# Optimization experiments

Hardware: AMD Instinct MI355X
Metric: run time of the kernel (lower is better)

The kernel has to match this reference:

```python
import jax, jax.numpy as jnp
import numpy as np

N_HEAD = 8
HEAD_DIM = 64
DIM = 512
INNER = N_HEAD * HEAD_DIM
ATT_THRESHOLD = 1e-4
SCALE = HEAD_DIM ** -0.5


def setup_inputs() -> dict:
    key = jax.random.key(0)
    ks = jax.random.split(key, 7)
    b, n, dn = 2, 2048, 2048
    fr = jax.random.normal(ks[0], (b, n, DIM), dtype=jnp.float32)
    dt = jax.random.normal(ks[1], (b, dn, DIM), dtype=jnp.float32)
    s = DIM ** -0.5
    Wq = jax.random.normal(ks[2], (DIM, INNER), dtype=jnp.float32) * s
    Wk = jax.random.normal(ks[3], (DIM, INNER), dtype=jnp.float32) * s
    Wv = jax.random.normal(ks[4], (DIM, INNER), dtype=jnp.float32) * s
    Wo = jax.random.normal(ks[5], (INNER, DIM), dtype=jnp.float32) * (INNER ** -0.5)
    bo = jax.random.normal(ks[6], (DIM,), dtype=jnp.float32) * 0.01
    return {"fr": fr, "dt": dt, "Wq": Wq, "Wk": Wk, "Wv": Wv, "Wo": Wo, "bo": bo}


def reference(fr, dt, Wq, Wk, Wv, Wo, bo):
    b, n, _ = fr.shape
    dn = dt.shape[1]
    # projections -> [b, seq, n_head, head_dim]
    q = (fr @ Wq).reshape(b, n, N_HEAD, HEAD_DIM)
    k = (dt @ Wk).reshape(b, dn, N_HEAD, HEAD_DIM)
    v = (dt @ Wv).reshape(b, dn, N_HEAD, HEAD_DIM)
    # full attention matrix [b, h, n, dn]
    scores = jnp.einsum('bihd,bjhd->bhij', q, k) * SCALE
    attn = jax.nn.softmax(scores, axis=-1)
    # torch .clip(t) with one positional arg clamps the MIN: max(attn, t)
    attn = jnp.maximum(attn, ATT_THRESHOLD) - ATT_THRESHOLD
    attn = attn / jnp.sum(attn, axis=-1, keepdims=True)
    out = jnp.einsum('bhij,bjhd->bihd', attn, v).reshape(b, n, INNER)
    return out @ Wo + bo
```

## Files before the change

### kernel.cpp

```cpp
#include <hip/hip_runtime.h>
#include <hip/hip_bf16.h>

#define BB 2
#define SEQ 2048
#define NHEAD 8
#define HD 64
#define ATT_T 1e-4f
#define QSCALE 0.18033688011112042f

typedef short s16x8 __attribute__((ext_vector_type(8)));
typedef float f32x16 __attribute__((ext_vector_type(16)));

#define MFMA32(a, b, c) __builtin_amdgcn_mfma_f32_32x32x16_bf16((a), (b), (c), 0, 0, 0)
#define EXP2(x) __builtin_amdgcn_exp2f(x)
#define SB0() __builtin_amdgcn_sched_barrier(0)
#define WAITVM0() __builtin_amdgcn_s_waitcnt(0x0F70)
#define WAITVM4() __builtin_amdgcn_s_waitcnt(0x0F74)
#define WAITVM8() __builtin_amdgcn_s_waitcnt(0x0F78)

__device__ __forceinline__ unsigned short bfr(float x) {
  __hip_bfloat16 h = __float2bfloat16(x);
  return __builtin_bit_cast(unsigned short, h);
}
__device__ __forceinline__ unsigned int packbf(float a, float b) {
  return (unsigned int)bfr(a) | ((unsigned int)bfr(b) << 16);
}
__device__ __forceinline__ unsigned int permpack(float a, float b) {
  return __builtin_amdgcn_perm(__builtin_bit_cast(unsigned int, b),
                               __builtin_bit_cast(unsigned int, a), 0x07060302u);
}
__device__ __forceinline__ void async16(const void* g, void* l) {
  __builtin_amdgcn_global_load_lds(
      (const __attribute__((address_space(1))) unsigned int*)g,
      (__attribute__((address_space(3))) unsigned int*)l, 16, 0, 0);
}

__global__ __launch_bounds__(256) void convT(const float* __restrict__ w0,
                                             const float* __restrict__ w1,
                                             const float* __restrict__ w2,
                                             const float* __restrict__ w3,
                                             unsigned short* __restrict__ o0,
                                             unsigned short* __restrict__ o1,
                                             unsigned short* __restrict__ o2,
                                             unsigned short* __restrict__ o3) {
  __shared__ float tle[64][65];
  const float* W = blockIdx.z == 0 ? w0 : blockIdx.z == 1 ? w1 : blockIdx.z == 2 ? w2 : w3;
  unsigned short* WT = blockIdx.z == 0 ? o0 : blockIdx.z == 1 ? o1 : blockIdx.z == 2 ? o2 : o3;
  const int r0 = blockIdx.y * 64, c0 = blockIdx.x * 64;
  const int tr = threadIdx.x >> 4;
  const int tc = threadIdx.x & 15;
  #pragma unroll
  for (int i = 0; i < 4; i++) {
    int r = tr + i * 16;
    float4 v = *(const float4*)(W + (size_t)(r0 + r) * 512 + c0 + tc * 4);
    tle[r][tc * 4 + 0] = v.x;
    tle[r][tc * 4 + 1] = v.y;
    tle[r][tc * 4 + 2] = v.z;
    tle[r][tc * 4 + 3] = v.w;
  }
  __syncthreads();
  #pragma unroll
  for (int i = 0; i < 4; i++) {
    int c = tr + i * 16;
    int rr = tc * 4;
    uint2 p;
    p.x = packbf(tle[rr + 0][c], tle[rr + 1][c]);
    p.y = packbf(tle[rr + 2][c], tle[rr + 3][c]);
    *(uint2*)(WT + (size_t)(c0 + c) * 512 + r0 + rr) = p;
  }
}

__global__ __launch_bounds__(256) void gemm_qkv(const float* __restrict__ frF,
                                                const float* __restrict__ dtF,
                                                const unsigned short* __restrict__ WqT,
                                                const unsigned short* __restrict__ WkT,
                                                const unsigned short* __restrict__ WvT,
                                                unsigned short* __restrict__ Qp,
                                                unsigned short* __restrict__ Kp,
                                                unsigned short* __restrict__ VTp) {
  __shared__ __align__(16) unsigned short smem[24576];
  unsigned short* Asm = smem;
  unsigned short* Bsm = smem + 8192;
  const int tid = threadIdx.x, lane = tid & 63, w = tid >> 6;
  const int l31 = lane & 31, lh = lane >> 5;
  const int m0 = blockIdx.y * 64, n0 = blockIdx.x * 128;
  const int z = blockIdx.z;
  const float* A = z == 0 ? frF : dtF;
  const unsigned short* BT = z == 0 ? WqT : (z == 1 ? WkT : WvT);
  unsigned short* OP = z == 0 ? Qp : (z == 1 ? Kp : VTp);
  const float scale = z == 0 ? QSCALE : 1.0f;

  const int arow = tid >> 2, aseg = tid & 3;
  const float* Ap = A + (size_t)(m0 + arow) * 512 + aseg * 16;
  const int aoff = (arow >> 5) * 2048 + aseg * 512 + (arow & 31) * 8;

  auto stageB = [&](int kt, int buf) {
    const int k0 = kt * 64;
    #pragma unroll
    for (int i = 0; i < 4; i++) {
      int r = w * 4 + i, gn = r >> 2, ks = r & 3;
      async16(BT + (size_t)(n0 + gn * 32 + l31) * 512 + k0 + ks * 16 + lh * 8,
              Bsm + buf * 8192 + r * 512);
    }
  };
  auto ldA = [&](int kt, float4* r4) {
    #pragma unroll
    for (int i = 0; i < 4; i++) r4[i] = *(const float4*)(Ap + kt * 64 + i * 4);
  };
  auto wrA = [&](int buf, const float4* r4) {
    uint4 w0v, w1v;
    w0v.x = packbf(r4[0].x, r4[0].y); w0v.y = packbf(r4[0].z, r4[0].w);
    w0v.z = packbf(r4[1].x, r4[1].y); w0v.w = packbf(r4[1].z, r4[1].w);
    w1v.x = packbf(r4[2].x, r4[2].y); w1v.y = packbf(r4[2].z, r4[2].w);
    w1v.z = packbf(r4[3].x, r4[3].y); w1v.w = packbf(r4[3].z, r4[3].w);
    *(uint4*)(Asm + buf * 4096 + aoff) = w0v;
    *(uint4*)(Asm + buf * 4096 + aoff + 256) = w1v;
  };

  f32x16 acc[2];
  #pragma unroll
  for (int j = 0; j < 2; j++)
    #pragma unroll
    for (int r = 0; r < 16; r++) acc[j][r] = 0.f;

  float4 areg[4];
  ldA(0, areg);
  stageB(0, 0);
  wrA(0, areg);
  ldA(1, areg);

  for (int kt = 0; kt < 8; ++kt) {
    __syncthreads();
    if (kt + 1 < 8) {
      const int nb = (kt + 1) & 1;
      stageB(kt + 1, nb);
      wrA(nb, areg);
      if (kt + 2 < 8) ldA(kt + 2, areg);
    }
    const int buf = kt & 1;
    const unsigned short* as = Asm + buf * 4096 + (w & 1) * 2048;
    const unsigned short* bs = Bsm + buf * 8192 + (w >> 1) * 4096;
    #pragma unroll
    for (int ks = 0; ks < 4; ++ks) {
      s16x8 af = *(const s16x8*)(as + ks * 512 + lane * 8);
      s16x8 b0 = *(const s16x8*)(bs + ks * 512 + lane * 8);
      s16x8 b1 = *(const s16x8*)(bs + 2048 + ks * 512 + lane * 8);
      acc[0] = MFMA32(af, b0, acc[0]);
      acc[1] = MFMA32(af, b1, acc[1]);
    }
  }

  const int wm = (w & 1) * 32, wn = (w >> 1) * 64;
  const int bb = m0 >> 11, s0 = m0 & 2047;
  __syncthreads();
  if (z <= 1) {
    #pragma unroll
    for (int j = 0; j < 2; j++)
      #pragma unroll
      for (int r = 0; r < 16; r++) {
        int mm = wm + (r & 3) + 8 * (r >> 2) + 4 * lh;
        int nn = wn + j * 32 + l31;
        smem[mm * 136 + nn] = bfr(acc[j][r] * scale);
      }
    __syncthreads();
    #pragma unroll
    for (int it = 0; it < 4; ++it) {
      int c = tid + it * 256;
      int mm = c >> 4, seg = c & 15;
      uint4 vdat = *(const uint4*)(smem + mm * 136 + seg * 8);
      int n = n0 + seg * 8, h = n >> 6, d = n & 63;
      *(uint4*)(OP + ((size_t)((bb * NHEAD + h) * SEQ + s0 + mm)) * HD + d) = vdat;
    }
  } else {
    #pragma unroll
    for (int j = 0; j < 2; j++)
      #pragma unroll
      for (int r = 0; r < 16; r += 2) {
        int mm = wm + (r & 3) + 8 * (r >> 2) + 4 * lh;
        int nn = wn + j * 32 + l31;
        *(unsigned int*)(smem + nn * 72 + mm) = packbf(acc[j][r], acc[j][r + 1]);
      }
    __syncthreads();
    #pragma unroll
    for (int it = 0; it < 4; ++it) {
      int c = tid + it * 256;
      int nn = c >> 3, seg = c & 7;
      uint4 vdat = *(const uint4*)(smem + nn * 72 + seg * 8);
      int n = n0 + nn, h = n >> 6, d = n & 63;
      *(uint4*)(OP + ((size_t)((bb * NHEAD + h) * HD + d)) * SEQ + s0 + seg * 8) = vdat;
    }
  }
}

__global__ __launch_bounds__(256) void gemm_out(const unsigned short* __restrict__ A,
                                                const unsigned short* __restrict__ BT,
                                                const float* __restrict__ bias,
                                                float* __restrict__ O) {
  __shared__ __align__(16) unsigned short smem[16384];
  unsigned short* Asm = smem;
  unsigned short* Bsm = smem + 8192;
  const int tid = threadIdx.x, lane = tid & 63, w = tid >> 6;
  const int l31 = lane & 31, lh = lane >> 5;
  const int m0 = blockIdx.y * 64, n0 = blockIdx.x * 64;

  auto stage = [&](int kt, int buf) {
    const int k0 = kt * 64;
    #pragma unroll
    for (int i = 0; i < 2; i++) {
      int r = w * 2 + i, g = r >> 2, ks = r & 3;
      async16(A + (size_t)(m0 + g * 32 + l31) * 512 + k0 + ks * 16 + lh * 8,
              Asm + buf * 4096 + r * 512);
      async16(BT + (size_t)(n0 + g * 32 + l31) * 512 + k0 + ks * 16 + lh * 8,
              Bsm + buf * 4096 + r * 512);
    }
  };

  f32x16 acc;
  #pragma unroll
  for (int r = 0; r < 16; r++) acc[r] = 0.f;

  stage(0, 0);
  for (int kt = 0; kt < 8; ++kt) {
    __syncthreads();
    if (kt + 1 < 8) stage(kt + 1, (kt + 1) & 1);
    const int buf = kt & 1;
    const unsigned short* as = Asm + buf * 4096 + (w & 1) * 2048;
    const unsigned short* bs = Bsm + buf * 4096 + (w >> 1) * 2048;
    #pragma unroll
    for (int ks = 0; ks < 4; ++ks) {
      s16x8 af = *(const s16x8*)(as + ks * 512 + lane * 8);
      s16x8 bf = *(const s16x8*)(bs + ks * 512 + lane * 8);
      acc = MFMA32(af, bf, acc);
    }
  }

  const int wm = (w & 1) * 32, wn = (w >> 1) * 32;
  float bv = bias[n0 + wn + l31];
  #pragma unroll
  for (int r = 0; r < 16; r++) {
    int mm = wm + (r & 3) + 8 * (r >> 2) + 4 * lh;
    O[(size_t)(m0 + mm) * 512 + n0 + wn + l31] = acc[r] + bv;
  }
}

__global__ __launch_bounds__(256, 2) void attn_mfma(const unsigned short* __restrict__ Q,
                                                    const unsigned short* __restrict__ K,
                                                    const unsigned short* __restrict__ VT,
                                                    unsigned short* __restrict__ O) {
  __shared__ __align__(16) unsigned short arena[4][8192];
  __shared__ float larr[4][64];
  __shared__ float warr[4][64];

  const int tid = threadIdx.x;
  const int lane = tid & 63;
  const int w = tid >> 6;
  const int l31 = lane & 31, lh = lane >> 5;

  const int bid = blockIdx.x;
  const int g = bid & 7, j = bid >> 3;
  const int bh = g * 2 + (j >> 5);
  const int qt = j & 31;

  const unsigned short* Qh = Q + (size_t)bh * SEQ * HD;
  const unsigned short* Kh = K + (size_t)bh * SEQ * HD;
  const unsigned short* VTh = VT + (size_t)bh * HD * SEQ;

  s16x8 qf[2][4];
  #pragma unroll
  for (int q2 = 0; q2 < 2; q2++)
    #pragma unroll
    for (int t = 0; t < 4; t++)
      qf[q2][t] = *(const s16x8*)(Qh + (size_t)(qt * 64 + q2 * 32 + l31) * HD + 16 * t + 8 * lh);

  unsigned short* kbuf = &arena[w][0];
  unsigned short* vbuf = &arena[w][4096];
  const int kbase = w * 512;

  auto stageK = [&](int c, int slot) {
    const unsigned short* base = Kh + (size_t)(kbase + c * 32 + l31) * HD + lh * 8;
    #pragma unroll
    for (int tt = 0; tt < 4; tt++)
      async16(base + tt * 16, kbuf + slot * 2048 + tt * 512);
  };
  auto stageV = [&](int c, int slot) {
    #pragma unroll
    for (int dh = 0; dh < 2; dh++)
      #pragma unroll
      for (int kc = 0; kc < 2; kc++)
        async16(VTh + (size_t)(dh * 32 + l31) * SEQ + kbase + c * 32 + kc * 16 + lh * 8,
                vbuf + slot * 2048 + (dh * 2 + kc) * 512);
  };

  float lsum[2] = {0.f, 0.f};
  f32x16 scp[2];

  auto accum_l = [&]() {
    #pragma unroll
    for (int q2 = 0; q2 < 2; q2++) {
      float s0 = 0.f, s1 = 0.f, s2 = 0.f, s3 = 0.f;
      #pragma unroll
      for (int r = 0; r < 4; r++) {
        s0 += EXP2(scp[q2][r]);
        s1 += EXP2(scp[q2][4 + r]);
        s2 += EXP2(scp[q2][8 + r]);
        s3 += EXP2(scp[q2][12 + r]);
      }
      lsum[q2] += (s0 + s1) + (s2 + s3);
    }
  };

  stageK(0, 0);
  for (int c = 0; c < 16; ++c) {
    const int slot = c & 1;
    if (c + 1 < 16) stageK(c + 1, slot ^ 1);
    if (c > 0) accum_l();
    if (c + 1 < 16) { WAITVM4(); } else { WAITVM0(); }
    SB0();
    s16x8 kf[4];
    #pragma unroll
    for (int tt = 0; tt < 4; tt++)
      kf[tt] = *(const s16x8*)(kbuf + slot * 2048 + tt * 512 + lane * 8);
    #pragma unroll
    for (int q2 = 0; q2 < 2; q2++) {
      f32x16 sc;
      #pragma unroll
      for (int r = 0; r < 16; r++) sc[r] = 0.f;
      #pragma unroll
      for (int tt = 0; tt < 4; tt++) sc = MFMA32(kf[tt], qf[q2][tt], sc);
      scp[q2] = sc;
    }
  }
  accum_l();
  #pragma unroll
  for (int q2 = 0; q2 < 2; q2++) lsum[q2] += __shfl_xor(lsum[q2], 32);
  if (lh == 0) { larr[w][l31] = lsum[0]; larr[w][32 + l31] = lsum[1]; }
  __syncthreads();
  float tl[2];
  #pragma unroll
  for (int q2 = 0; q2 < 2; q2++)
    tl[q2] = ATT_T * (larr[0][q2 * 32 + l31] + larr[1][q2 * 32 + l31] +
                      larr[2][q2 * 32 + l31] + larr[3][q2 * 32 + l31]);

  f32x16 acc[2][2];
  #pragma unroll
  for (int q2 = 0; q2 < 2; q2++)
    #pragma unroll
    for (int dh = 0; dh < 2; dh++)
      #pragma unroll
      for (int r = 0; r < 16; r++) acc[q2][dh][r] = 0.f;
  float wacc[2] = {0.f, 0.f};
  s16x8 vfp[2][2];

  auto softmax_pv = [&]() {
    s16x8 pf[2][2];
    #pragma unroll
    for (int q2 = 0; q2 < 2; q2++) {
      uint2 quads[4];
      #pragma unroll
      for (int gq = 0; gq < 4; gq++) {
        float u0 = fmaxf(EXP2(scp[q2][4 * gq + 0]) - tl[q2], 0.f);
        float u1 = fmaxf(EXP2(scp[q2][4 * gq + 1]) - tl[q2], 0.f);
        float u2 = fmaxf(EXP2(scp[q2][4 * gq + 2]) - tl[q2], 0.f);
        float u3 = fmaxf(EXP2(scp[q2][4 * gq + 3]) - tl[q2], 0.f);
        wacc[q2] += (u0 + u1) + (u2 + u3);
        quads[gq].x = permpack(u0, u1);
        quads[gq].y = permpack(u2, u3);
      }
      #pragma unroll
      for (int tp = 0; tp < 2; tp++) {
        uint2 ea, eb;
        ea.x = (unsigned)__shfl_xor((int)quads[2 * tp].x, 32);
        ea.y = (unsigned)__shfl_xor((int)quads[2 * tp].y, 32);
        eb.x = (unsigned)__shfl_xor((int)quads[2 * tp + 1].x, 32);
        eb.y = (unsigned)__shfl_xor((int)quads[2 * tp + 1].y, 32);
        uint4 fr;
        if (lh == 0) { fr.x = quads[2 * tp].x; fr.y = quads[2 * tp].y; fr.z = ea.x; fr.w = ea.y; }
        else         { fr.x = eb.x; fr.y = eb.y; fr.z = quads[2 * tp + 1].x; fr.w = quads[2 * tp + 1].y; }
        pf[q2][tp] = __builtin_bit_cast(s16x8, fr);
      }
    }
    #pragma unroll
    for (int q2 = 0; q2 < 2; q2++)
      #pragma unroll
      for (int dh = 0; dh < 2; dh++) {
        acc[q2][dh] = MFMA32(pf[q2][0], vfp[dh][0], acc[q2][dh]);
        acc[q2][dh] = MFMA32(pf[q2][1], vfp[dh][1], acc[q2][dh]);
      }
  };

  stageK(0, 0);
  stageV(0, 0);
  for (int c = 0; c < 16; ++c) {
    const int slot = c & 1;
    if (c + 1 < 16) { stageK(c + 1, slot ^ 1); stageV(c + 1, slot ^ 1); }
    if (c > 0) softmax_pv();
    if (c + 1 < 16) { WAITVM8(); } else { WAITVM0(); }
    SB0();
    s16x8 kf[4];
    #pragma unroll
    for (int tt = 0; tt < 4; tt++)
      kf[tt] = *(const s16x8*)(kbuf + slot * 2048 + tt * 512 + lane * 8);
    #pragma unroll
    for (int dh = 0; dh < 2; dh++)
      #pragma unroll
      for (int kc = 0; kc < 2; kc++)
        vfp[dh][kc] = *(const s16x8*)(vbuf + slot * 2048 + (dh * 2 + kc) * 512 + lane * 8);
    #pragma unroll
    for (int q2 = 0; q2 < 2; q2++) {
      f32x16 sc;
      #pragma unroll
      for (int r = 0; r < 16; r++) sc[r] = 0.f;
      #pragma unroll
      for (int tt = 0; tt < 4; tt++) sc = MFMA32(kf[tt], qf[q2][tt], sc);
      scp[q2] = sc;
    }
  }
  softmax_pv();

  #pragma unroll
  for (int q2 = 0; q2 < 2; q2++) wacc[q2] += __shfl_xor(wacc[q2], 32);
  if (lh == 0) { warr[w][l31] = wacc[0]; warr[w][32 + l31] = wacc[1]; }
  __syncthreads();

  float* plane0 = (float*)&arena[0][0];
  float* plane1 = (float*)&arena[2][0];

  if (w >= 2) {
    float* pl = (w == 2) ? plane0 : plane1;
    #pragma unroll
    for (int q2 = 0; q2 < 2; q2++)
      #pragma unroll
      for (int dh = 0; dh < 2; dh++)
        #pragma unroll
        for (int r = 0; r < 16; r++) {
          int ql = q2 * 32 + (r & 3) + 8 * (r >> 2) + 4 * lh;
          pl[ql * 64 + dh * 32 + l31] = acc[q2][dh][r];
        }
  }
  __syncthreads();
  if (w < 2) {
    float* pl = (w == 0) ? plane0 : plane1;
    #pragma unroll
    for (int q2 = 0; q2 < 2; q2++)
      #pragma unroll
      for (int dh = 0; dh < 2; dh++)
        #pragma unroll
        for (int r = 0; r < 16; r++) {
          int ql = q2 * 32 + (r & 3) + 8 * (r >> 2) + 4 * lh;
          acc[q2][dh][r] += pl[ql * 64 + dh * 32 + l31];
        }
  }
  __syncthreads();
  if (w == 1) {
    #pragma unroll
    for (int q2 = 0; q2 < 2; q2++)
      #pragma unroll
      for (int dh = 0; dh < 2; dh++)
        #pragma unroll
        for (int r = 0; r < 16; r++) {
          int ql = q2 * 32 + (r & 3) + 8 * (r >> 2) + 4 * lh;
          plane0[ql * 64 + dh * 32 + l31] = acc[q2][dh][r];
        }
  }
  __syncthreads();
  unsigned short* otile = &arena[2][0];
  if (w == 0) {
    #pragma unroll
    for (int q2 = 0; q2 < 2; q2++)
      #pragma unroll
      for (int dh = 0; dh < 2; dh++)
        #pragma unroll
        for (int r = 0; r < 16; r++) {
          int ql = q2 * 32 + (r & 3) + 8 * (r >> 2) + 4 * lh;
          float wt = warr[0][ql] + warr[1][ql] + warr[2][ql] + warr[3][ql];
          float v = (acc[q2][dh][r] + plane0[ql * 64 + dh * 32 + l31]) / wt;
          otile[ql * 64 + dh * 32 + l31] = bfr(v);
        }
  }
  __syncthreads();
  const int b = bh >> 3, h = bh & 7;
  #pragma unroll
  for (int it = 0; it < 2; ++it) {
    int c2 = tid + it * 256;
    int mm = c2 >> 3, seg = c2 & 7;
    uint4 vdat = *(const uint4*)(otile + mm * 64 + seg * 8);
    *(uint4*)(O + ((size_t)(b * SEQ + qt * 64 + mm)) * 512 + h * HD + seg * 8) = vdat;
  }
}

extern "C" void kernel_launch(void* const* d_in, const int* in_sizes, int n_in,
                              void* d_out, int out_size, void* d_ws, size_t ws_size,
                              hipStream_t stream) {
  const float* fr = (const float*)d_in[0];
  const float* dt = (const float*)d_in[1];
  const float* Wq = (const float*)d_in[2];
  const float* Wk = (const float*)d_in[3];
  const float* Wv = (const float*)d_in[4];
  const float* Wo = (const float*)d_in[5];
  const float* bo = (const float*)d_in[6];
  float* out = (float*)d_out;

  const size_t planeE = (size_t)BB * SEQ * 512;
  const size_t wE = 512 * 512;
  unsigned short* p = (unsigned short*)d_ws;
  unsigned short* WqT = p; p += wE;
  unsigned short* WkT = p; p += wE;
  unsigned short* WvT = p; p += wE;
  unsigned short* WoT = p; p += wE;
  unsigned short* Qp  = p; p += planeE;
  unsigned short* Kp  = p; p += planeE;
  unsigned short* VTp = p; p += planeE;
  unsigned short* aoB = p; p += planeE;

  convT<<<dim3(8, 8, 4), 256, 0, stream>>>(Wq, Wk, Wv, Wo, WqT, WkT, WvT, WoT);

  gemm_qkv<<<dim3(4, 64, 3), 256, 0, stream>>>(fr, dt, WqT, WkT, WvT, Qp, Kp, VTp);

  attn_mfma<<<BB * NHEAD * 32, 256, 0, stream>>>(Qp, Kp, VTp, aoB);

  gemm_out<<<dim3(8, 64), 256, 0, stream>>>(aoB, WoT, bo, out);
}
```

Before: 162.8 us.

## Halve attention query tile to 32 rows, single-buffer K/V, raise occupancy

The attention kernel now handles 32 query rows per block instead of 64, doubling the grid and shrinking per-wave accumulators and LDS to about half. The double-buffered K/V staging is replaced with one buffer: each iteration waits for the loads, reads fragments into registers, waits on LDS, then issues the next async load before the MFMA and softmax work. Launch bounds rise to 4 blocks per CU to gain occupancy and latency hiding. In exchange, K/V are re-read from global/L2 twice as often and the per-wave software pipeline gives way to inter-wave overlap.

```diff
diff --git a/kernel.cpp b/kernel.cpp
--- a/kernel.cpp
+++ b/kernel.cpp
@@ -14,9 +14,8 @@
 #define MFMA32(a, b, c) __builtin_amdgcn_mfma_f32_32x32x16_bf16((a), (b), (c), 0, 0, 0)
 #define EXP2(x) __builtin_amdgcn_exp2f(x)
 #define SB0() __builtin_amdgcn_sched_barrier(0)
-#define WAITVM0() __builtin_amdgcn_s_waitcnt(0x0F70)
-#define WAITVM4() __builtin_amdgcn_s_waitcnt(0x0F74)
-#define WAITVM8() __builtin_amdgcn_s_waitcnt(0x0F78)
+#define WAITVM0()   __builtin_amdgcn_s_waitcnt(0x0F70)
+#define WAITLGKM0() __builtin_amdgcn_s_waitcnt(0xC07F)
 
 __device__ __forceinline__ unsigned short bfr(float x) {
   __hip_bfloat16 h = __float2bfloat16(x);
@@ -243,13 +242,13 @@
   }
 }
 
-__global__ __launch_bounds__(256, 2) void attn_mfma(const unsigned short* __restrict__ Q,
+__global__ __launch_bounds__(256, 4) void attn_mfma(const unsigned short* __restrict__ Q,
                                                     const unsigned short* __restrict__ K,
                                                     const unsigned short* __restrict__ VT,
                                                     unsigned short* __restrict__ O) {
-  __shared__ __align__(16) unsigned short arena[4][8192];
-  __shared__ float larr[4][64];
-  __shared__ float warr[4][64];
+  __shared__ __align__(16) unsigned short arena[4][4096];
+  __shared__ float larr[4][32];
+  __shared__ float warr[4][32];
 
   const int tid = threadIdx.x;
   const int lane = tid & 63;
@@ -258,233 +257,185 @@
 
   const int bid = blockIdx.x;
   const int g = bid & 7, j = bid >> 3;
-  const int bh = g * 2 + (j >> 5);
-  const int qt = j & 31;
+  const int bh = g * 2 + (j >> 6);
+  const int qt = j & 63;
 
   const unsigned short* Qh = Q + (size_t)bh * SEQ * HD;
   const unsigned short* Kh = K + (size_t)bh * SEQ * HD;
   const unsigned short* VTh = VT + (size_t)bh * HD * SEQ;
 
-  s16x8 qf[2][4];
-  #pragma unroll
-  for (int q2 = 0; q2 < 2; q2++)
-    #pragma unroll
-    for (int t = 0; t < 4; t++)
-      qf[q2][t] = *(const s16x8*)(Qh + (size_t)(qt * 64 + q2 * 32 + l31) * HD + 16 * t + 8 * lh);
+  s16x8 qf[4];
+  #pragma unroll
+  for (int t = 0; t < 4; t++)
+    qf[t] = *(const s16x8*)(Qh + (size_t)(qt * 32 + l31) * HD + 16 * t + 8 * lh);
 
   unsigned short* kbuf = &arena[w][0];
-  unsigned short* vbuf = &arena[w][4096];
+  unsigned short* vbuf = &arena[w][2048];
   const int kbase = w * 512;
 
-  auto stageK = [&](int c, int slot) {
+  auto stageK = [&](int c) {
     const unsigned short* base = Kh + (size_t)(kbase + c * 32 + l31) * HD + lh * 8;
     #pragma unroll
     for (int tt = 0; tt < 4; tt++)
-      async16(base + tt * 16, kbuf + slot * 2048 + tt * 512);
-  };
-  auto stageV = [&](int c, int slot) {
+      async16(base + tt * 16, kbuf + tt * 512);
+  };
+  auto stageV = [&](int c) {
     #pragma unroll
     for (int dh = 0; dh < 2; dh++)
       #pragma unroll
       for (int kc = 0; kc < 2; kc++)
         async16(VTh + (size_t)(dh * 32 + l31) * SEQ + kbase + c * 32 + kc * 16 + lh * 8,
-                vbuf + slot * 2048 + (dh * 2 + kc) * 512);
-  };
-
-  float lsum[2] = {0.f, 0.f};
-  f32x16 scp[2];
-
-  auto accum_l = [&]() {
-    #pragma unroll
-    for (int q2 = 0; q2 < 2; q2++) {
-      float s0 = 0.f, s1 = 0.f, s2 = 0.f, s3 = 0.f;
-      #pragma unroll
-      for (int r = 0; r < 4; r++) {
-        s0 += EXP2(scp[q2][r]);
-        s1 += EXP2(scp[q2][4 + r]);
-        s2 += EXP2(scp[q2][8 + r]);
-        s3 += EXP2(scp[q2][12 + r]);
-      }
-      lsum[q2] += (s0 + s1) + (s2 + s3);
-    }
-  };
-
-  stageK(0, 0);
+                vbuf + (dh * 2 + kc) * 512);
+  };
+
+  float lsum = 0.f;
+  stageK(0);
   for (int c = 0; c < 16; ++c) {
-    const int slot = c & 1;
-    if (c + 1 < 16) stageK(c + 1, slot ^ 1);
-    if (c > 0) accum_l();
-    if (c + 1 < 16) { WAITVM4(); } else { WAITVM0(); }
+    WAITVM0();
     SB0();
     s16x8 kf[4];
     #pragma unroll
     for (int tt = 0; tt < 4; tt++)
-      kf[tt] = *(const s16x8*)(kbuf + slot * 2048 + tt * 512 + lane * 8);
-    #pragma unroll
-    for (int q2 = 0; q2 < 2; q2++) {
-      f32x16 sc;
-      #pragma unroll
-      for (int r = 0; r < 16; r++) sc[r] = 0.f;
-      #pragma unroll
-      for (int tt = 0; tt < 4; tt++) sc = MFMA32(kf[tt], qf[q2][tt], sc);
-      scp[q2] = sc;
-    }
-  }
-  accum_l();
-  #pragma unroll
-  for (int q2 = 0; q2 < 2; q2++) lsum[q2] += __shfl_xor(lsum[q2], 32);
-  if (lh == 0) { larr[w][l31] = lsum[0]; larr[w][32 + l31] = lsum[1]; }
-  __syncthreads();
-  float tl[2];
-  #pragma unroll
-  for (int q2 = 0; q2 < 2; q2++)
-    tl[q2] = ATT_T * (larr[0][q2 * 32 + l31] + larr[1][q2 * 32 + l31] +
-                      larr[2][q2 * 32 + l31] + larr[3][q2 * 32 + l31]);
-
-  f32x16 acc[2][2];
-  #pragma unroll
-  for (int q2 = 0; q2 < 2; q2++)
-    #pragma unroll
-    for (int dh = 0; dh < 2; dh++)
-      #pragma unroll
-      for (int r = 0; r < 16; r++) acc[q2][dh][r] = 0.f;
-  float wacc[2] = {0.f, 0.f};
-  s16x8 vfp[2][2];
-
-  auto softmax_pv = [&]() {
-    s16x8 pf[2][2];
-    #pragma unroll
-    for (int q2 = 0; q2 < 2; q2++) {
-      uint2 quads[4];
-      #pragma unroll
-      for (int gq = 0; gq < 4; gq++) {
-        float u0 = fmaxf(EXP2(scp[q2][4 * gq + 0]) - tl[q2], 0.f);
-        float u1 = fmaxf(EXP2(scp[q2][4 * gq + 1]) - tl[q2], 0.f);
-        float u2 = fmaxf(EXP2(scp[q2][4 * gq + 2]) - tl[q2], 0.f);
-        float u3 = fmaxf(EXP2(scp[q2][4 * gq + 3]) - tl[q2], 0.f);
-        wacc[q2] += (u0 + u1) + (u2 + u3);
-        quads[gq].x = permpack(u0, u1);
-        quads[gq].y = permpack(u2, u3);
-      }
-      #pragma unroll
-      for (int tp = 0; tp < 2; tp++) {
-        uint2 ea, eb;
-        ea.x = (unsigned)__shfl_xor((int)quads[2 * tp].x, 32);
-        ea.y = (unsigned)__shfl_xor((int)quads[2 * tp].y, 32);
-        eb.x = (unsigned)__shfl_xor((int)quads[2 * tp + 1].x, 32);
-        eb.y = (unsigned)__shfl_xor((int)quads[2 * tp + 1].y, 32);
-        uint4 fr;
-        if (lh == 0) { fr.x = quads[2 * tp].x; fr.y = quads[2 * tp].y; fr.z = ea.x; fr.w = ea.y; }
-        else         { fr.x = eb.x; fr.y = eb.y; fr.z = quads[2 * tp + 1].x; fr.w = quads[2 * tp + 1].y; }
-        pf[q2][tp] = __builtin_bit_cast(s16x8, fr);
-      }
-    }
-    #pragma unroll
-    for (int q2 = 0; q2 < 2; q2++)
-      #pragma unroll
-      for (int dh = 0; dh < 2; dh++) {
-        acc[q2][dh] = MFMA32(pf[q2][0], vfp[dh][0], acc[q2][dh]);
-        acc[q2][dh] = MFMA32(pf[q2][1], vfp[dh][1], acc[q2][dh]);
-      }
-  };
-
-  stageK(0, 0);
-  stageV(0, 0);
+      kf[tt] = *(const s16x8*)(kbuf + tt * 512 + lane * 8);
+    WAITLGKM0();
+    SB0();
+    if (c + 1 < 16) stageK(c + 1);
+    f32x16 sc;
+    #pragma unroll
+    for (int r = 0; r < 16; r++) sc[r] = 0.f;
+    #pragma unroll
+    for (int tt = 0; tt < 4; tt++) sc = MFMA32(kf[tt], qf[tt], sc);
+    float s0 = 0.f, s1 = 0.f, s2 = 0.f, s3 = 0.f;
+    #pragma unroll
+    for (int r = 0; r < 4; r++) {
+      s0 += EXP2(sc[r]);
+      s1 += EXP2(sc[4 + r]);
+      s2 += EXP2(sc[8 + r]);
+      s3 += EXP2(sc[12 + r]);
+    }
+    lsum += (s0 + s1) + (s2 + s3);
+  }
+  lsum += __shfl_xor(lsum, 32);
+  if (lh == 0) larr[w][l31] = lsum;
+  __syncthreads();
+  const float tl = ATT_T * (larr[0][l31] + larr[1][l31] + larr[2][l31] + larr[3][l31]);
+
+  f32x16 acc[2];
+  #pragma unroll
+  for (int dh = 0; dh < 2; dh++)
+    #pragma unroll
+    for (int r = 0; r < 16; r++) acc[dh][r] = 0.f;
+  float wacc = 0.f;
+
+  stageK(0);
+  stageV(0);
   for (int c = 0; c < 16; ++c) {
-    const int slot = c & 1;
-    if (c + 1 < 16) { stageK(c + 1, slot ^ 1); stageV(c + 1, slot ^ 1); }
-    if (c > 0) softmax_pv();
-    if (c + 1 < 16) { WAITVM8(); } else { WAITVM0(); }
+    WAITVM0();
     SB0();
-    s16x8 kf[4];
+    s16x8 kf[4], vf[2][2];
     #pragma unroll
     for (int tt = 0; tt < 4; tt++)
-      kf[tt] = *(const s16x8*)(kbuf + slot * 2048 + tt * 512 + lane * 8);
+      kf[tt] = *(const s16x8*)(kbuf + tt * 512 + lane * 8);
     #pragma unroll
     for (int dh = 0; dh < 2; dh++)
       #pragma unroll
       for (int kc = 0; kc < 2; kc++)
-        vfp[dh][kc] = *(const s16x8*)(vbuf + slot * 2048 + (dh * 2 + kc) * 512 + lane * 8);
-    #pragma unroll
-    for (int q2 = 0; q2 < 2; q2++) {
-      f32x16 sc;
-      #pragma unroll
-      for (int r = 0; r < 16; r++) sc[r] = 0.f;
-      #pragma unroll
-      for (int tt = 0; tt < 4; tt++) sc = MFMA32(kf[tt], qf[q2][tt], sc);
-      scp[q2] = sc;
-    }
-  }
-  softmax_pv();
-
-  #pragma unroll
-  for (int q2 = 0; q2 < 2; q2++) wacc[q2] += __shfl_xor(wacc[q2], 32);
-  if (lh == 0) { warr[w][l31] = wacc[0]; warr[w][32 + l31] = wacc[1]; }
+        vf[dh][kc] = *(const s16x8*)(vbuf + (dh * 2 + kc) * 512 + lane * 8);
+    WAITLGKM0();
+    SB0();
+    if (c + 1 < 16) { stageK(c + 1); stageV(c + 1); }
+    f32x16 sc;
+    #pragma unroll
+    for (int r = 0; r < 16; r++) sc[r] = 0.f;
+    #pragma unroll
+    for (int tt = 0; tt < 4; tt++) sc = MFMA32(kf[tt], qf[tt], sc);
+    uint2 quads[4];
+    #pragma unroll
+    for (int gq = 0; gq < 4; gq++) {
+      float u0 = fmaxf(EXP2(sc[4 * gq + 0]) - tl, 0.f);
+      float u1 = fmaxf(EXP2(sc[4 * gq + 1]) - tl, 0.f);
+      float u2 = fmaxf(EXP2(sc[4 * gq + 2]) - tl, 0.f);
+      float u3 = fmaxf(EXP2(sc[4 * gq + 3]) - tl, 0.f);
+      wacc += (u0 + u1) + (u2 + u3);
+      quads[gq].x = permpack(u0, u1);
+      quads[gq].y = permpack(u2, u3);
+    }
+    s16x8 pf[2];
+    #pragma unroll
+    for (int tp = 0; tp < 2; tp++) {
+      unsigned sx = (lh == 0) ? quads[2 * tp + 1].x : quads[2 * tp].x;
+      unsigned sy = (lh == 0) ? quads[2 * tp + 1].y : quads[2 * tp].y;
+      unsigned rx = (unsigned)__shfl_xor((int)sx, 32);
+      unsigned ry = (unsigned)__shfl_xor((int)sy, 32);
+      uint4 fr;
+      if (lh == 0) { fr.x = quads[2 * tp].x; fr.y = quads[2 * tp].y; fr.z = rx; fr.w = ry; }
+      else         { fr.x = rx; fr.y = ry; fr.z = quads[2 * tp + 1].x; fr.w = quads[2 * tp + 1].y; }
+      pf[tp] = __builtin_bit_cast(s16x8, fr);
+    }
+    #pragma unroll
+    for (int dh = 0; dh < 2; dh++) {
+      acc[dh] = MFMA32(pf[0], vf[dh][0], acc[dh]);
+      acc[dh] = MFMA32(pf[1], vf[dh][1], acc[dh]);
+    }
+  }
+
+  wacc += __shfl_xor(wacc, 32);
+  if (lh == 0) warr[w][l31] = wacc;
   __syncthreads();
 
   float* plane0 = (float*)&arena[0][0];
-  float* plane1 = (float*)&arena[2][0];
+  float* plane1 = (float*)&arena[1][0];
+  unsigned short* otile = &arena[2][0];
 
   if (w >= 2) {
     float* pl = (w == 2) ? plane0 : plane1;
     #pragma unroll
-    for (int q2 = 0; q2 < 2; q2++)
-      #pragma unroll
-      for (int dh = 0; dh < 2; dh++)
-        #pragma unroll
-        for (int r = 0; r < 16; r++) {
-          int ql = q2 * 32 + (r & 3) + 8 * (r >> 2) + 4 * lh;
-          pl[ql * 64 + dh * 32 + l31] = acc[q2][dh][r];
-        }
+    for (int dh = 0; dh < 2; dh++)
+      #pragma unroll
+      for (int r = 0; r < 16; r++) {
+        int ql = (r & 3) + 8 * (r >> 2) + 4 * lh;
+        pl[ql * 64 + dh * 32 + l31] = acc[dh][r];
+      }
   }
   __syncthreads();
   if (w < 2) {
     float* pl = (w == 0) ? plane0 : plane1;
     #pragma unroll
-    for (int q2 = 0; q2 < 2; q2++)
-      #pragma unroll
-      for (int dh = 0; dh < 2; dh++)
-        #pragma unroll
-        for (int r = 0; r < 16; r++) {
-          int ql = q2 * 32 + (r & 3) + 8 * (r >> 2) + 4 * lh;
-          acc[q2][dh][r] += pl[ql * 64 + dh * 32 + l31];
-        }
+    for (int dh = 0; dh < 2; dh++)
+      #pragma unroll
+      for (int r = 0; r < 16; r++) {
+        int ql = (r & 3) + 8 * (r >> 2) + 4 * lh;
+        acc[dh][r] += pl[ql * 64 + dh * 32 + l31];
+      }
   }
   __syncthreads();
   if (w == 1) {
     #pragma unroll
-    for (int q2 = 0; q2 < 2; q2++)
-      #pragma unroll
-      for (int dh = 0; dh < 2; dh++)
-        #pragma unroll
-        for (int r = 0; r < 16; r++) {
-          int ql = q2 * 32 + (r & 3) + 8 * (r >> 2) + 4 * lh;
-          plane0[ql * 64 + dh * 32 + l31] = acc[q2][dh][r];
-        }
-  }
-  __syncthreads();
-  unsigned short* otile = &arena[2][0];
+    for (int dh = 0; dh < 2; dh++)
+      #pragma unroll
+      for (int r = 0; r < 16; r++) {
+        int ql = (r & 3) + 8 * (r >> 2) + 4 * lh;
+        plane0[ql * 64 + dh * 32 + l31] = acc[dh][r];
+      }
+  }
+  __syncthreads();
   if (w == 0) {
     #pragma unroll
-    for (int q2 = 0; q2 < 2; q2++)
-      #pragma unroll
-      for (int dh = 0; dh < 2; dh++)
-        #pragma unroll
-        for (int r = 0; r < 16; r++) {
-          int ql = q2 * 32 + (r & 3) + 8 * (r >> 2) + 4 * lh;
-          float wt = warr[0][ql] + warr[1][ql] + warr[2][ql] + warr[3][ql];
-          float v = (acc[q2][dh][r] + plane0[ql * 64 + dh * 32 + l31]) / wt;
-          otile[ql * 64 + dh * 32 + l31] = bfr(v);
-        }
+    for (int dh = 0; dh < 2; dh++)
+      #pragma unroll
+      for (int r = 0; r < 16; r++) {
+        int ql = (r & 3) + 8 * (r >> 2) + 4 * lh;
+        float wt = warr[0][ql] + warr[1][ql] + warr[2][ql] + warr[3][ql];
+        float v = (acc[dh][r] + plane0[ql * 64 + dh * 32 + l31]) / wt;
+        otile[ql * 64 + dh * 32 + l31] = bfr(v);
+      }
   }
   __syncthreads();
   const int b = bh >> 3, h = bh & 7;
-  #pragma unroll
-  for (int it = 0; it < 2; ++it) {
-    int c2 = tid + it * 256;
-    int mm = c2 >> 3, seg = c2 & 7;
+  {
+    int mm = tid >> 3, seg = tid & 7;
     uint4 vdat = *(const uint4*)(otile + mm * 64 + seg * 8);
-    *(uint4*)(O + ((size_t)(b * SEQ + qt * 64 + mm)) * 512 + h * HD + seg * 8) = vdat;
+    *(uint4*)(O + ((size_t)(b * SEQ + qt * 32 + mm)) * 512 + h * HD + seg * 8) = vdat;
   }
 }
 
@@ -516,7 +467,7 @@
 
   gemm_qkv<<<dim3(4, 64, 3), 256, 0, stream>>>(fr, dt, WqT, WkT, WvT, Qp, Kp, VTp);
 
-  attn_mfma<<<BB * NHEAD * 32, 256, 0, stream>>>(Qp, Kp, VTp, aoB);
+  attn_mfma<<<BB * NHEAD * 64, 256, 0, stream>>>(Qp, Kp, VTp, aoB);
 
   gemm_out<<<dim3(8, 64), 256, 0, stream>>>(aoB, WoT, bo, out);
 }
```

New measurement: 202.2 us. 24.2% more time.
